# Kernel tuning notes

Measured on AMD Instinct MI355X. Metric: run time of the kernel, lower is better.

## Reference

```python
import jax, jax.numpy as jnp
import numpy as np

B, T, D = 256, 128, 64
H, A, O = 512, 128, 32


def setup_inputs() -> dict:
    key = jax.random.key(0)
    ks = jax.random.split(key, 16)
    u = lambda k, sh, lo, hi: jax.random.uniform(k, sh, jnp.float32, lo, hi)
    return {
        "x_states": jax.random.normal(ks[0], (B, T, D), jnp.float32),
        "x_dts": jax.random.uniform(ks[1], (B, T), jnp.float32) * 0.1,
        # StepwiseAttention params (stored [in, out])
        "Wq": u(ks[2], (D, A), -0.1, 0.1), "bq": u(ks[3], (A,), -0.1, 0.1),
        "Wk": u(ks[4], (H, A), -0.1, 0.1), "bk": u(ks[5], (A,), -0.1, 0.1),
        "Wv": u(ks[6], (H, A), -0.1, 0.1), "bv": u(ks[7], (A,), -0.1, 0.1),
        # LTCAttentionCell params
        "W_gd": u(ks[8], (D + H + A, 2 * H), -0.1, 0.1),
        "b_gd": u(ks[9], (2 * H,), -0.1, 0.1),
        "W_tau": u(ks[10], (H, H), -0.1, 0.1),
        "b_tau": u(ks[11], (H,), -0.1, 0.1),
        "gleak": u(ks[12], (H,), 0.001, 1.0),
        "cm": u(ks[13], (H,), 0.4, 0.6),
        # output head
        "W_fc": u(ks[14], (H, O), -0.1, 0.1),
        "b_fc": u(ks[15], (O,), -0.1, 0.1),
    }


def _forward(x_states, x_dts, Wq, bq, Wk, bk, Wv, bv,
             W_gd, b_gd, W_tau, b_tau, gleak, cm, W_fc, b_fc):
    scale = jnp.sqrt(jnp.asarray(A, jnp.float32))
    leak = jax.nn.softplus(cm) + jax.nn.softplus(gleak)  # [H]

    def dhdt(h, x_t, ctx):
        combined = jnp.concatenate([x_t, h, ctx], axis=1)        # [B, D+H+A]
        gd = combined @ W_gd + b_gd                              # [B, 2H]
        gate, dyn = jnp.split(gd, 2, axis=1)
        tau = jax.nn.softplus(h @ W_tau + b_tau)                 # [B, H]
        num = jax.nn.sigmoid(gate) * jnp.tanh(dyn) - h
        return num / (tau + leak + 1e-6)

    def step(carry, inp):
        h, hist = carry            # h [B,H], hist [B,T,H]
        t, x_t, dt = inp           # t scalar, x_t [B,D], dt [B]
        # stepwise attention over history h_1..h_t
        Q = x_t @ Wq + bq                                        # [B, A]
        K = hist @ Wk + bk                                       # [B, T, A]
        V = hist @ Wv + bv                                       # [B, T, A]
        scores = jnp.einsum('ba,bta->bt', Q, K) / scale          # [B, T]
        valid = jnp.arange(T) < t
        scores = jnp.where(valid[None, :], scores, -1e9)
        w = jax.nn.softmax(scores, axis=-1)
        ctx = jnp.einsum('bt,bta->ba', w, V)
        ctx = jnp.where(t > 0, ctx, jnp.zeros_like(ctx))         # empty history -> 0
        # one RK4 step (torchdiffeq 'rk4' = 3/8-rule variant), step size dt per sample
        dtc = dt[:, None]
        k1 = dhdt(h, x_t, ctx)
        k2 = dhdt(h + dtc * k1 / 3.0, x_t, ctx)
        k3 = dhdt(h + dtc * (k2 - k1 / 3.0), x_t, ctx)
        k4 = dhdt(h + dtc * (k1 - k2 + k3), x_t, ctx)
        h_next = h + dtc * (k1 + 3.0 * k2 + 3.0 * k3 + k4) / 8.0
        hist = jax.lax.dynamic_update_slice(hist, h_next[:, None, :], (0, t, 0))
        return (h_next, hist), None

    h0 = jnp.zeros((B, H), jnp.float32)
    hist0 = jnp.zeros((B, T, H), jnp.float32)
    xs = (jnp.arange(T), jnp.swapaxes(x_states, 0, 1), jnp.swapaxes(x_dts, 0, 1))
    (h_final, _), _ = jax.lax.scan(step, (h0, hist0), xs)
    return h_final @ W_fc + b_fc                                 # [B, O]


def reference(x_states, x_dts, Wq, bq, Wk, bk, Wv, bv,
              W_gd, b_gd, W_tau, b_tau, gleak, cm, W_fc, b_fc):
    return _forward(x_states, x_dts, Wq, bq, Wk, bk, Wv, bv,
                    W_gd, b_gd, W_tau, b_tau, gleak, cm, W_fc, b_fc)
```

## Files before the change

kernel.cpp:

```cpp
#include <hip/hip_runtime.h>
#include <math.h>

#define B_ 256
#define T_ 128
#define D_ 64
#define H_ 512
#define A_ 128
#define O_ 32

typedef __attribute__((ext_vector_type(8))) short short8;
typedef __attribute__((ext_vector_type(8))) unsigned short ushort8;
typedef __attribute__((ext_vector_type(4))) float floatx4;
typedef __attribute__((ext_vector_type(4))) unsigned int uintx4;
typedef unsigned long long ull;

__device__ __forceinline__ float sp_(float x) {
    return fmaxf(x, 0.f) + log1pf(expf(-fabsf(x)));
}
__device__ __forceinline__ float sigm_(float x) {
    return 1.f / (1.f + expf(-x));
}
__device__ __forceinline__ unsigned short f2bf_(float f) {
    unsigned int u = __float_as_uint(f);
    return (unsigned short)((u + 0x7FFFu + ((u >> 16) & 1u)) >> 16);
}
__device__ __forceinline__ float bf2f_(unsigned short u) {
    return __uint_as_float(((unsigned)u) << 16);
}

__device__ __forceinline__ void ld16sc(uintx4& d, const void* p) {
    asm volatile("global_load_dwordx4 %0, %1, off sc0 sc1"
                 : "=v"(d) : "v"(p) : "memory");
}
__device__ __forceinline__ void ld4sc(float& d, const void* p) {
    asm volatile("global_load_dword %0, %1, off sc0 sc1"
                 : "=v"(d) : "v"(p) : "memory");
}
__device__ __forceinline__ void ld4su(unsigned& d, const void* p) {
    asm volatile("global_load_dword %0, %1, off sc0 sc1"
                 : "=v"(d) : "v"(p) : "memory");
}
__device__ __forceinline__ void st64sc(ull* p, ull v) {
    asm volatile("global_store_dwordx2 %0, %1, off sc0 sc1"
                 :: "v"(p), "v"(v) : "memory");
}
__device__ __forceinline__ void stu32sc(unsigned* p, unsigned v) {
    asm volatile("global_store_dword %0, %1, off sc0 sc1"
                 :: "v"(p), "v"(v) : "memory");
}
__device__ __forceinline__ void vmwait4(uintx4& a, uintx4& b, uintx4& c,
                                        uintx4& d) {
    asm volatile("s_waitcnt vmcnt(0)"
                 : "+v"(a), "+v"(b), "+v"(c), "+v"(d)::"memory");
}
__device__ __forceinline__ void vmwait8(uintx4& a, uintx4& b, uintx4& c,
                                        uintx4& d, uintx4& e, uintx4& f,
                                        uintx4& g, uintx4& h) {
    asm volatile("s_waitcnt vmcnt(0)"
                 : "+v"(a), "+v"(b), "+v"(c), "+v"(d), "+v"(e), "+v"(f),
                   "+v"(g), "+v"(h)::"memory");
}
__device__ __forceinline__ void vmwait16f(float& a0, float& a1, float& a2,
                                          float& a3, float& a4, float& a5,
                                          float& a6, float& a7, float& b0,
                                          float& b1, float& b2, float& b3,
                                          float& b4, float& b5, float& b6,
                                          float& b7) {
    asm volatile("s_waitcnt vmcnt(0)"
                 : "+v"(a0), "+v"(a1), "+v"(a2), "+v"(a3), "+v"(a4), "+v"(a5),
                   "+v"(a6), "+v"(a7), "+v"(b0), "+v"(b1), "+v"(b2), "+v"(b3),
                   "+v"(b4), "+v"(b5), "+v"(b6), "+v"(b7)::"memory");
}
__device__ __forceinline__ void vmwait8u(unsigned& a, unsigned& b, unsigned& c,
                                         unsigned& d, unsigned& e, unsigned& f,
                                         unsigned& g, unsigned& h) {
    asm volatile("s_waitcnt vmcnt(0)"
                 : "+v"(a), "+v"(b), "+v"(c), "+v"(d), "+v"(e), "+v"(f),
                   "+v"(g), "+v"(h)::"memory");
}
__device__ __forceinline__ void vmwait4u(unsigned& a, unsigned& b, unsigned& c,
                                         unsigned& d) {
    asm volatile("s_waitcnt vmcnt(0)"
                 : "+v"(a), "+v"(b), "+v"(c), "+v"(d)::"memory");
}
__device__ __forceinline__ void vmwait1u(unsigned& a) {
    asm volatile("s_waitcnt vmcnt(0)" : "+v"(a)::"memory");
}
__device__ __forceinline__ floatx4 u2f_(uintx4 u) {
    union { uintx4 u; floatx4 f; } c;
    c.u = u;
    return c.f;
}
__device__ __forceinline__ void stf_(float* p, float v) {
    __hip_atomic_store(p, v, __ATOMIC_RELAXED, __HIP_MEMORY_SCOPE_SYSTEM);
}

__global__ void init_kernel(unsigned short* __restrict__ hpack,
                            unsigned* __restrict__ bar) {
    int i = blockIdx.x * 256 + threadIdx.x;
    if (i < B_ * H_) hpack[i] = 0;
    if (i < 18432) bar[i] = 0u;
}

__global__ void pack_w_kernel(const float* __restrict__ W_gd,
                              const float* __restrict__ W_tau,
                              const float* __restrict__ Wk,
                              const float* __restrict__ Wv,
                              unsigned short* __restrict__ Wpack) {
    int gid = blockIdx.x * 256 + threadIdx.x;
    if (gid >= 1114112) return;
    int j = gid & 7;
    int l = (gid >> 3) & 63;
    int kpart = (l >> 4) * 8 + j;
    int npart = l & 15;
    float v;
    if (gid < 786432) {
        int f = gid >> 9;
        int s = f % 3;
        int rem = f / 3;
        int kb = rem & 15, ct = rem >> 4;
        int k = kb * 32 + kpart;
        int c = ct * 16 + npart;
        if (s == 0)      v = W_gd[(size_t)(D_ + k) * 1024 + c];
        else if (s == 1) v = W_gd[(size_t)(D_ + k) * 1024 + 512 + c];
        else             v = W_tau[(size_t)k * 512 + c];
    } else if (gid < 851968) {
        int r = gid - 786432;
        int f = r >> 9;
        int s = f & 1, kb = (f >> 1) & 1, ct = f >> 2;
        int k = kb * 32 + kpart;
        int c = ct * 16 + npart;
        v = W_gd[(size_t)k * 1024 + s * 512 + c];
    } else if (gid < 983040) {
        int r = gid - 851968;
        int f = r >> 9;
        int s = f & 1, kb = (f >> 1) & 3, ct = f >> 3;
        int k = kb * 32 + kpart;
        int c = ct * 16 + npart;
        v = W_gd[(size_t)(D_ + H_ + k) * 1024 + s * 512 + c];
    } else {
        int r = gid - 983040;
        int f = r >> 9;
        int kb = f & 15, c4 = f >> 4;
        int k = kb * 32 + kpart;
        int n = (c4 & 7) * 16 + npart;
        v = (c4 < 8) ? Wk[(size_t)k * A_ + n] : Wv[(size_t)k * A_ + n];
    }
    Wpack[gid] = f2bf_(v);
}

__device__ __forceinline__ void gsyncF(unsigned* flags, int j, unsigned cnt) {
    asm volatile("s_waitcnt vmcnt(0)" ::: "memory");
    __syncthreads();
    if (threadIdx.x == 0) stu32sc(flags + j * 64, cnt);
    if (threadIdx.x < 8) {
        unsigned v;
        do {
            ld4su(v, flags + threadIdx.x * 64);
            vmwait1u(v);
            if (v >= cnt) break;
            __builtin_amdgcn_s_sleep(1);
        } while (true);
    }
    __syncthreads();
}

struct P {
    const float *x, *dts, *Wq, *bq, *bk, *bv, *b_gd, *b_tau, *gleak, *cm,
        *W_fc, *b_fc;
    float *h, *ctx, *out, *Kpart, *Vpart;
    unsigned short* Kh;
    const unsigned short *Wy, *Wx, *Wc, *Wkv;
    unsigned short *hpack, *yapack, *ybpack, *ycpack;
    unsigned* bar;
};

__global__ __launch_bounds__(256, 1) void fused_kernel(P p) {
    const int tid = threadIdx.x;
    const int bid = blockIdx.x;
    const int lane = tid & 63;
    const int wave = tid >> 6;
    const int g = bid & 15;
    const int j = bid >> 4;
    const int ct = j * 4 + wave;
    unsigned* flags = p.bar + g * 512;
    unsigned* senbase = p.bar + 8192;
    #define SEN(kind, src) (senbase + (((kind)*16 + g) * 8 + (src)) * 16)

    __shared__ float WqL[D_ * 129];
    __shared__ float xs4[2][D_];
    __shared__ float q4[2][A_];
    __shared__ float sc4[2][T_];
    __shared__ float red[2][2];
    __shared__ __align__(16) unsigned short AsL[32 * 256];
    __shared__ __align__(16) unsigned short ypbuf[4 * 256];
    __shared__ __align__(16) unsigned short As2[2 * 512];
    __shared__ unsigned short VhL[2][A_][136];

    const int quad = lane >> 4;
    const int c = ct * 16 + (lane & 15);
    const float btau = p.b_tau[c];
    const float lk = sp_(p.cm[c]) + sp_(p.gleak[c]) + 1e-6f;
    const float bgd_g = p.b_gd[c];
    const float bgd_d = p.b_gd[512 + c];
    const int aoff = (quad >> 1) * 256 + (lane & 15) * 16 + (quad & 1) * 8;
    const int ypw = wave * 256 + (lane & 15);

    const int sub = tid >> 7;
    const int tl = tid & 127;
    const int r = g * 16 + j * 2 + sub;
    const int rrow = r & 15;

    short8 wg[16], wd[16], wt[16];
    short8 wxg[2], wxd[2], wcg[4], wcd[4];
    {
        const short8* Wy8 = (const short8*)p.Wy;
        #pragma unroll
        for (int kb = 0; kb < 16; ++kb) {
            wg[kb] = Wy8[((ct * 16 + kb) * 3 + 0) * 64 + lane];
            wd[kb] = Wy8[((ct * 16 + kb) * 3 + 1) * 64 + lane];
            wt[kb] = Wy8[((ct * 16 + kb) * 3 + 2) * 64 + lane];
        }
        const short8* Wx8 = (const short8*)p.Wx;
        const short8* Wc8 = (const short8*)p.Wc;
        #pragma unroll
        for (int kb = 0; kb < 2; ++kb) {
            wxg[kb] = Wx8[((ct * 2 + kb) * 2 + 0) * 64 + lane];
            wxd[kb] = Wx8[((ct * 2 + kb) * 2 + 1) * 64 + lane];
        }
        #pragma unroll
        for (int kb = 0; kb < 4; ++kb) {
            wcg[kb] = Wc8[((ct * 4 + kb) * 2 + 0) * 64 + lane];
            wcd[kb] = Wc8[((ct * 4 + kb) * 2 + 1) * 64 + lane];
        }
    }

    for (int i = tid; i < D_ * A_; i += 256) {
        int d = i >> 7, a = i & 127;
        WqL[d * 129 + a] = p.Wq[i];
    }

    floatx4 hreg = {0.f, 0.f, 0.f, 0.f};
    floatx4 rk1, rk2, rk3, baseg, based, ycur, dt4;

    const short8* Wkv8 = (const short8*)p.Wkv;

    __syncthreads();

    for (int t = 0; t < T_; ++t) {
        {
            float kk[8], vv[8];
            uintx4 av[4];
            {
                const unsigned short* src = p.hpack + g * 8192;
                const unsigned expv = (unsigned)t;
                unsigned s0, s1, s2, s3, s4, s5, s6, s7;
                for (;;) {
                    #pragma unroll
                    for (int jj = 0; jj < 8; ++jj) {
                        ld4sc(kk[jj],
                              p.Kpart + ((g * 8 + jj) * 16 + rrow) * 128 + tl);
                        ld4sc(vv[jj],
                              p.Vpart + ((g * 8 + jj) * 16 + rrow) * 128 + tl);
                    }
                    #pragma unroll
                    for (int i = 0; i < 4; ++i)
                        ld16sc(av[i], src + (size_t)tid * 8 + i * 2048);
                    ld4su(s0, SEN(4, 0)); ld4su(s1, SEN(4, 1));
                    ld4su(s2, SEN(4, 2)); ld4su(s3, SEN(4, 3));
                    ld4su(s4, SEN(4, 4)); ld4su(s5, SEN(4, 5));
                    ld4su(s6, SEN(4, 6)); ld4su(s7, SEN(4, 7));
                    vmwait16f(kk[0], kk[1], kk[2], kk[3], kk[4], kk[5], kk[6],
                              kk[7], vv[0], vv[1], vv[2], vv[3], vv[4], vv[5],
                              vv[6], vv[7]);
                    vmwait4(av[0], av[1], av[2], av[3]);
                    vmwait8u(s0, s1, s2, s3, s4, s5, s6, s7);
                    if (s0 >= expv && s1 >= expv && s2 >= expv && s3 >= expv &&
                        s4 >= expv && s5 >= expv && s6 >= expv && s7 >= expv)
                        break;
                    __builtin_amdgcn_s_sleep(1);
                }
            }
            #pragma unroll
            for (int i = 0; i < 4; ++i)
                ((uintx4*)AsL)[tid + i * 256] = av[i];
            if (t > 0) {
                float ks = p.bk[tl], vs = p.bv[tl];
                #pragma unroll
                for (int jj = 0; jj < 8; ++jj) {
                    ks += kk[jj];
                    vs += vv[jj];
                }
                p.Kh[(size_t)(r * T_ + (t - 1)) * A_ + tl] = f2bf_(ks);
                VhL[sub][tl][t - 1] = f2bf_(vs);
            }
            if (tl < 16)
                ((float4*)xs4[sub])[tl] =
                    ((const float4*)&p.x[(r * T_ + t) * D_])[tl];
            __syncthreads();
            float qa = p.bq[tl];
            #pragma unroll 8
            for (int d = 0; d < D_; ++d) qa += xs4[sub][d] * WqL[d * 129 + tl];
            q4[sub][tl] = qa;
            __syncthreads();
            if (t == 0) {
                stf_(p.ctx + r * A_ + tl, 0.f);
            } else {
                const float rscale = 0.08838834764831845f;
                const int grp = tl >> 4, ln = tl & 15;
                float qv[8];
                #pragma unroll
                for (int i = 0; i < 8; ++i) qv[i] = q4[sub][ln * 8 + i];
                for (int s = grp; s < t; s += 8) {
                    ushort8 k8 = *((const ushort8*)(p.Kh +
                                     (size_t)(r * T_ + s) * A_) + ln);
                    float a2 = 0.f;
                    #pragma unroll
                    for (int i = 0; i < 8; ++i) a2 += bf2f_(k8[i]) * qv[i];
                    #pragma unroll
                    for (int off = 8; off > 0; off >>= 1)
                        a2 += __shfl_xor(a2, off, 16);
                    if (ln == 0) sc4[sub][s] = a2 * rscale;
                }
                __syncthreads();
                float mloc = -1e30f;
                for (int s = tl; s < t; s += 128)
                    mloc = fmaxf(mloc, sc4[sub][s]);
                #pragma unroll
                for (int off = 32; off > 0; off >>= 1)
                    mloc = fmaxf(mloc, __shfl_xor(mloc, off, 64));
                if (lane == 0) red[sub][wave & 1] = mloc;
                __syncthreads();
                float m = fmaxf(red[sub][0], red[sub][1]);
                float ssum = 0.f;
                for (int s = tl; s < t; s += 128) {
                    float e = expf(sc4[sub][s] - m);
                    sc4[sub][s] = e;
                    ssum += e;
                }
                #pragma unroll
                for (int off = 32; off > 0; off >>= 1)
                    ssum += __shfl_xor(ssum, off, 64);
                __syncthreads();
                if (lane == 0) red[sub][wave & 1] = ssum;
                __syncthreads();
                float rs = 1.f / (red[sub][0] + red[sub][1]);
                const unsigned short* Vrow = &VhL[sub][tl][0];
                float ca0 = 0.f, ca1 = 0.f;
                int s0 = 0;
                for (; s0 + 16 <= t; s0 += 16) {
                    ushort8 v0 = *(const ushort8*)(Vrow + s0);
                    ushort8 v1 = *(const ushort8*)(Vrow + s0 + 8);
                    #pragma unroll
                    for (int i = 0; i < 8; ++i) {
                        ca0 += sc4[sub][s0 + i] * bf2f_(v0[i]);
                        ca1 += sc4[sub][s0 + 8 + i] * bf2f_(v1[i]);
                    }
                }
                if (s0 + 8 <= t) {
                    ushort8 v0 = *(const ushort8*)(Vrow + s0);
                    #pragma unroll
                    for (int i = 0; i < 8; ++i)
                        ca0 += sc4[sub][s0 + i] * bf2f_(v0[i]);
                    s0 += 8;
                }
                for (; s0 < t; ++s0) ca0 += sc4[sub][s0] * bf2f_(Vrow[s0]);
                stf_(p.ctx + r * A_ + tl, (ca0 + ca1) * rs);
            }
        }
        asm volatile("s_waitcnt vmcnt(0)" ::: "memory");
        __syncthreads();
        if (tid == 0) stu32sc(SEN(0, j), (unsigned)(t + 1));

        {
            const int mrow = lane & 15;
            const float* crow = &p.ctx[(g * 16 + mrow) * A_];
            uintx4 cc[8];
            {
                const unsigned* senp = SEN(0, mrow >> 1);
                const unsigned expv = (unsigned)(t + 1);
                unsigned sv;
                for (;;) {
                    #pragma unroll
                    for (int kb = 0; kb < 4; ++kb) {
                        ld16sc(cc[2 * kb], crow + kb * 32 + quad * 8);
                        ld16sc(cc[2 * kb + 1], crow + kb * 32 + quad * 8 + 4);
                    }
                    ld4su(sv, senp);
                    vmwait8(cc[0], cc[1], cc[2], cc[3], cc[4], cc[5], cc[6],
                            cc[7]);
                    vmwait1u(sv);
                    if (sv >= expv) break;
                    __builtin_amdgcn_s_sleep(1);
                }
            }
            #pragma unroll
            for (int i = 0; i < 4; ++i)
                dt4[i] = p.dts[(g * 16 + quad * 4 + i) * T_ + t];

            floatx4 bg = {0.f, 0.f, 0.f, 0.f};
            floatx4 bd = {0.f, 0.f, 0.f, 0.f};
            const float4* xrow =
                (const float4*)&p.x[((g * 16 + mrow) * T_ + t) * D_];
            #pragma unroll
            for (int kb = 0; kb < 2; ++kb) {
                float4 u = xrow[kb * 8 + quad * 2], v = xrow[kb * 8 + quad * 2 + 1];
                short8 ax;
                ax[0] = (short)f2bf_(u.x); ax[1] = (short)f2bf_(u.y);
                ax[2] = (short)f2bf_(u.z); ax[3] = (short)f2bf_(u.w);
                ax[4] = (short)f2bf_(v.x); ax[5] = (short)f2bf_(v.y);
                ax[6] = (short)f2bf_(v.z); ax[7] = (short)f2bf_(v.w);
                bg = __builtin_amdgcn_mfma_f32_16x16x32_bf16(ax, wxg[kb], bg, 0, 0, 0);
                bd = __builtin_amdgcn_mfma_f32_16x16x32_bf16(ax, wxd[kb], bd, 0, 0, 0);
            }
            #pragma unroll
            for (int kb = 0; kb < 4; ++kb) {
                floatx4 f0 = u2f_(cc[2 * kb]), f1 = u2f_(cc[2 * kb + 1]);
                short8 ac;
                ac[0] = (short)f2bf_(f0[0]); ac[1] = (short)f2bf_(f0[1]);
                ac[2] = (short)f2bf_(f0[2]); ac[3] = (short)f2bf_(f0[3]);
                ac[4] = (short)f2bf_(f1[0]); ac[5] = (short)f2bf_(f1[1]);
                ac[6] = (short)f2bf_(f1[2]); ac[7] = (short)f2bf_(f1[3]);
                bg = __builtin_amdgcn_mfma_f32_16x16x32_bf16(ac, wcg[kb], bg, 0, 0, 0);
                bd = __builtin_amdgcn_mfma_f32_16x16x32_bf16(ac, wcd[kb], bd, 0, 0, 0);
            }
            floatx4 ag = {0.f, 0.f, 0.f, 0.f};
            floatx4 ad = {0.f, 0.f, 0.f, 0.f};
            floatx4 at = {0.f, 0.f, 0.f, 0.f};
            #pragma unroll
            for (int kb = 0; kb < 16; ++kb) {
                short8 a = *(const short8*)(AsL + kb * 512 + aoff);
                ag = __builtin_amdgcn_mfma_f32_16x16x32_bf16(a, wg[kb], ag, 0, 0, 0);
                ad = __builtin_amdgcn_mfma_f32_16x16x32_bf16(a, wd[kb], ad, 0, 0, 0);
                at = __builtin_amdgcn_mfma_f32_16x16x32_bf16(a, wt[kb], at, 0, 0, 0);
            }
            #pragma unroll
            for (int i = 0; i < 4; ++i) {
                baseg[i] = bg[i] + bgd_g;
                based[i] = bd[i] + bgd_d;
                float gate = ag[i] + baseg[i];
                float dyn = ad[i] + based[i];
                float tau = sp_(at[i] + btau);
                float ki = (sigm_(gate) * tanhf(dyn) - hreg[i]) / (tau + lk);
                rk1[i] = ki;
                float yn = hreg[i] + dt4[i] * ki * (1.f / 3.f);
                ycur[i] = yn;
                ypbuf[ypw + (quad * 4 + i) * 16] = f2bf_(yn);
            }
            __syncthreads();
            st64sc((ull*)p.yapack + g * 2048 + j * 256 + tid,
                   ((const ull*)ypbuf)[tid]);
        }
        asm volatile("s_waitcnt vmcnt(0)" ::: "memory");
        __syncthreads();
        if (tid == 0) stu32sc(SEN(1, j), (unsigned)(t + 1));

        #pragma unroll 1
        for (int stage = 2; stage <= 4; ++stage) {
            const unsigned short* ysrc =
                (stage == 2) ? p.yapack : (stage == 3) ? p.ybpack : p.ycpack;
            unsigned short* ydst =
                (stage == 2) ? p.ybpack : (stage == 3) ? p.ycpack : p.hpack;
            const int senk = stage - 1;
            {
                const unsigned short* src = ysrc + g * 8192;
                const unsigned expv = (unsigned)(t + 1);
                const int sb = tid >> 7;
                uintx4 av[4];
                unsigned s0, s1, s2, s3;
                for (;;) {
                    #pragma unroll
                    for (int i = 0; i < 4; ++i)
                        ld16sc(av[i], src + (size_t)tid * 8 + i * 2048);
                    ld4su(s0, SEN(senk, sb + 0));
                    ld4su(s1, SEN(senk, sb + 2));
                    ld4su(s2, SEN(senk, sb + 4));
                    ld4su(s3, SEN(senk, sb + 6));
                    vmwait4(av[0], av[1], av[2], av[3]);
                    vmwait4u(s0, s1, s2, s3);
                    if (s0 >= expv && s1 >= expv && s2 >= expv && s3 >= expv)
                        break;
                    __builtin_amdgcn_s_sleep(1);
                }
                #pragma unroll
                for (int i = 0; i < 4; ++i)
                    ((uintx4*)AsL)[tid + i * 256] = av[i];
            }
            __syncthreads();
            floatx4 ag = {0.f, 0.f, 0.f, 0.f};
            floatx4 ad = {0.f, 0.f, 0.f, 0.f};
            floatx4 at = {0.f, 0.f, 0.f, 0.f};
            #pragma unroll
            for (int kb = 0; kb < 16; ++kb) {
                short8 a = *(const short8*)(AsL + kb * 512 + aoff);
                ag = __builtin_amdgcn_mfma_f32_16x16x32_bf16(a, wg[kb], ag, 0, 0, 0);
                ad = __builtin_amdgcn_mfma_f32_16x16x32_bf16(a, wd[kb], ad, 0, 0, 0);
                at = __builtin_amdgcn_mfma_f32_16x16x32_bf16(a, wt[kb], at, 0, 0, 0);
            }
            const int lane_p = ((c >> 3) & 3) * 16;
            #pragma unroll
            for (int i = 0; i < 4; ++i) {
                float gate = ag[i] + baseg[i];
                float dyn = ad[i] + based[i];
                float tau = sp_(at[i] + btau);
                float ki = (sigm_(gate) * tanhf(dyn) - ycur[i]) / (tau + lk);
                float yn;
                if (stage == 2) {
                    rk2[i] = ki;
                    yn = hreg[i] + dt4[i] * (ki - rk1[i] * (1.f / 3.f));
                } else if (stage == 3) {
                    rk3[i] = ki;
                    yn = hreg[i] + dt4[i] * (rk1[i] - rk2[i] + ki);
                } else {
                    yn = hreg[i] +
                         dt4[i] * (rk1[i] + 3.f * rk2[i] + 3.f * rk3[i] + ki) * 0.125f;
                    hreg[i] = yn;
                }
                ycur[i] = yn;
                ypbuf[ypw + (quad * 4 + i) * 16] = f2bf_(yn);
                if (stage == 4)
                    As2[(wave >> 1) * 512 + (c & 7) +
                        (lane_p + quad * 4 + i) * 8] = f2bf_(yn);
            }
            __syncthreads();
            st64sc((ull*)ydst + g * 2048 + j * 256 + tid,
                   ((const ull*)ypbuf)[tid]);
            if (stage == 4) {
                #pragma unroll
                for (int h4 = 0; h4 < 4; ++h4) {
                    const int c4 = wave + h4 * 4;
                    floatx4 acc = {0.f, 0.f, 0.f, 0.f};
                    #pragma unroll
                    for (int kk2 = 0; kk2 < 2; ++kk2) {
                        short8 a = *(const short8*)(As2 + (kk2 * 64 + lane) * 8);
                        acc = __builtin_amdgcn_mfma_f32_16x16x32_bf16(
                            a, Wkv8[(c4 * 16 + (j * 2 + kk2)) * 64 + lane], acc,
                            0, 0, 0);
                    }
                    const int ac = (c4 & 7) * 16 + (lane & 15);
                    float* part = (c4 < 8) ? p.Kpart : p.Vpart;
                    #pragma unroll
                    for (int i = 0; i < 4; ++i)
                        stf_(part + ((g * 8 + j) * 16 + quad * 4 + i) * 128 + ac,
                             acc[i]);
                }
            }
            asm volatile("s_waitcnt vmcnt(0)" ::: "memory");
            __syncthreads();
            if (tid == 0) stu32sc(SEN(stage, j), (unsigned)(t + 1));
        }
    }

    #pragma unroll
    for (int i = 0; i < 4; ++i)
        stf_(p.h + (g * 16 + quad * 4 + i) * H_ + c, hreg[i]);
    gsyncF(flags, j, 1u);
    {
        const int o = tl & 31, ks = tl >> 5;
        float acc = 0.f;
        const float* hrow = p.h + r * H_ + ks * 128;
        const float* wcol = p.W_fc + ks * 128 * O_ + o;
        #pragma unroll 1
        for (int rd = 0; rd < 4; ++rd) {
            uintx4 hh[8];
            #pragma unroll
            for (int i = 0; i < 8; ++i)
                ld16sc(hh[i], hrow + rd * 32 + i * 4);
            vmwait8(hh[0], hh[1], hh[2], hh[3], hh[4], hh[5], hh[6], hh[7]);
            #pragma unroll
            for (int i = 0; i < 8; ++i) {
                floatx4 f = u2f_(hh[i]);
                #pragma unroll
                for (int e = 0; e < 4; ++e)
                    acc += f[e] * wcol[(rd * 32 + i * 4 + e) * O_];
            }
        }
        sc4[sub][tl] = acc;
        __syncthreads();
        if (ks == 0)
            p.out[r * O_ + o] = acc + sc4[sub][o + 32] + sc4[sub][o + 64] +
                                sc4[sub][o + 96] + p.b_fc[o];
    }
    #undef SEN
}

extern "C" void kernel_launch(void* const* d_in, const int* in_sizes, int n_in,
                              void* d_out, int out_size, void* d_ws,
                              size_t ws_size, hipStream_t stream) {
    (void)in_sizes; (void)n_in; (void)out_size; (void)ws_size;
    P p;
    p.x = (const float*)d_in[0];
    p.dts = (const float*)d_in[1];
    p.Wq = (const float*)d_in[2];
    p.bq = (const float*)d_in[3];
    const float* Wk = (const float*)d_in[4];
    p.bk = (const float*)d_in[5];
    const float* Wv = (const float*)d_in[6];
    p.bv = (const float*)d_in[7];
    const float* W_gd = (const float*)d_in[8];
    p.b_gd = (const float*)d_in[9];
    const float* W_tau = (const float*)d_in[10];
    p.b_tau = (const float*)d_in[11];
    p.gleak = (const float*)d_in[12];
    p.cm = (const float*)d_in[13];
    p.W_fc = (const float*)d_in[14];
    p.b_fc = (const float*)d_in[15];
    p.out = (float*)d_out;

    float* ws = (float*)d_ws;
    p.h = ws;
    p.ctx = p.h + B_ * H_;
    p.Kpart = p.ctx + B_ * A_;
    p.Vpart = p.Kpart + 262144;
    unsigned short* Wpack = (unsigned short*)(p.Vpart + 262144);
    p.Wy = Wpack;
    p.Wx = Wpack + 786432;
    p.Wc = Wpack + 851968;
    p.Wkv = Wpack + 983040;
    p.hpack = Wpack + 1114112;
    p.yapack = p.hpack + B_ * H_;
    p.ybpack = p.yapack + B_ * H_;
    p.ycpack = p.ybpack + B_ * H_;
    p.Kh = p.ycpack + B_ * H_;
    p.bar = (unsigned*)(p.Kh + (size_t)B_ * T_ * A_);

    init_kernel<<<512, 256, 0, stream>>>(p.hpack, p.bar);
    pack_w_kernel<<<4352, 256, 0, stream>>>(W_gd, W_tau, Wk, Wv, Wpack);

    fused_kernel<<<dim3(128), dim3(256), 0, stream>>>(p);
}
```

Before: 3.542 ms.

## Halve persistent block count with 512-thread blocks and move V history to global

The persistent fused kernel now runs 64 blocks of 512 threads (8 waves) instead of 128 blocks of 256, so each block owns twice as many hidden columns and batch rows. This halves the number of producer blocks that every consumer must poll through the sentinel flags and partial K/V buffers, which should cut the per-step cross-block synchronisation and reduction cost. To free LDS, the bf16 V history moves from shared memory to a global buffer, and the context sum reads it with strided scalar loads. That adds global traffic and latency in the attention loop, and fewer blocks means less total parallelism.

Result: slower. 8.395 ms (+137.0%).

```diff
diff --git a/kernel.cpp b/kernel.cpp
--- a/kernel.cpp
+++ b/kernel.cpp
@@ -48,10 +48,8 @@
     asm volatile("global_store_dword %0, %1, off sc0 sc1"
                  :: "v"(p), "v"(v) : "memory");
 }
-__device__ __forceinline__ void vmwait4(uintx4& a, uintx4& b, uintx4& c,
-                                        uintx4& d) {
-    asm volatile("s_waitcnt vmcnt(0)"
-                 : "+v"(a), "+v"(b), "+v"(c), "+v"(d)::"memory");
+__device__ __forceinline__ void vmwait2(uintx4& a, uintx4& b) {
+    asm volatile("s_waitcnt vmcnt(0)" : "+v"(a), "+v"(b)::"memory");
 }
 __device__ __forceinline__ void vmwait8(uintx4& a, uintx4& b, uintx4& c,
                                         uintx4& d, uintx4& e, uintx4& f,
@@ -60,28 +58,20 @@
                  : "+v"(a), "+v"(b), "+v"(c), "+v"(d), "+v"(e), "+v"(f),
                    "+v"(g), "+v"(h)::"memory");
 }
-__device__ __forceinline__ void vmwait16f(float& a0, float& a1, float& a2,
-                                          float& a3, float& a4, float& a5,
-                                          float& a6, float& a7, float& b0,
-                                          float& b1, float& b2, float& b3,
-                                          float& b4, float& b5, float& b6,
-                                          float& b7) {
+__device__ __forceinline__ void vmwait8f(float& a0, float& a1, float& a2,
+                                         float& a3, float& a4, float& a5,
+                                         float& a6, float& a7) {
     asm volatile("s_waitcnt vmcnt(0)"
                  : "+v"(a0), "+v"(a1), "+v"(a2), "+v"(a3), "+v"(a4), "+v"(a5),
-                   "+v"(a6), "+v"(a7), "+v"(b0), "+v"(b1), "+v"(b2), "+v"(b3),
-                   "+v"(b4), "+v"(b5), "+v"(b6), "+v"(b7)::"memory");
-}
-__device__ __forceinline__ void vmwait8u(unsigned& a, unsigned& b, unsigned& c,
-                                         unsigned& d, unsigned& e, unsigned& f,
-                                         unsigned& g, unsigned& h) {
-    asm volatile("s_waitcnt vmcnt(0)"
-                 : "+v"(a), "+v"(b), "+v"(c), "+v"(d), "+v"(e), "+v"(f),
-                   "+v"(g), "+v"(h)::"memory");
+                   "+v"(a6), "+v"(a7)::"memory");
 }
 __device__ __forceinline__ void vmwait4u(unsigned& a, unsigned& b, unsigned& c,
                                          unsigned& d) {
     asm volatile("s_waitcnt vmcnt(0)"
                  : "+v"(a), "+v"(b), "+v"(c), "+v"(d)::"memory");
+}
+__device__ __forceinline__ void vmwait2u(unsigned& a, unsigned& b) {
+    asm volatile("s_waitcnt vmcnt(0)" : "+v"(a), "+v"(b)::"memory");
 }
 __device__ __forceinline__ void vmwait1u(unsigned& a) {
     asm volatile("s_waitcnt vmcnt(0)" : "+v"(a)::"memory");
@@ -153,7 +143,7 @@
     asm volatile("s_waitcnt vmcnt(0)" ::: "memory");
     __syncthreads();
     if (threadIdx.x == 0) stu32sc(flags + j * 64, cnt);
-    if (threadIdx.x < 8) {
+    if (threadIdx.x < 4) {
         unsigned v;
         do {
             ld4su(v, flags + threadIdx.x * 64);
@@ -169,33 +159,32 @@
     const float *x, *dts, *Wq, *bq, *bk, *bv, *b_gd, *b_tau, *gleak, *cm,
         *W_fc, *b_fc;
     float *h, *ctx, *out, *Kpart, *Vpart;
-    unsigned short* Kh;
+    unsigned short *Kh, *Vh;
     const unsigned short *Wy, *Wx, *Wc, *Wkv;
     unsigned short *hpack, *yapack, *ybpack, *ycpack;
     unsigned* bar;
 };
 
-__global__ __launch_bounds__(256, 1) void fused_kernel(P p) {
+__global__ __launch_bounds__(512, 2) void fused_kernel(P p) {
     const int tid = threadIdx.x;
     const int bid = blockIdx.x;
     const int lane = tid & 63;
     const int wave = tid >> 6;
     const int g = bid & 15;
     const int j = bid >> 4;
-    const int ct = j * 4 + wave;
+    const int ct = j * 8 + wave;
     unsigned* flags = p.bar + g * 512;
     unsigned* senbase = p.bar + 8192;
     #define SEN(kind, src) (senbase + (((kind)*16 + g) * 8 + (src)) * 16)
 
     __shared__ float WqL[D_ * 129];
-    __shared__ float xs4[2][D_];
-    __shared__ float q4[2][A_];
-    __shared__ float sc4[2][T_];
-    __shared__ float red[2][2];
+    __shared__ float xs4[4][D_];
+    __shared__ float q4[4][A_];
+    __shared__ float sc4[4][T_];
+    __shared__ float red[4][2];
     __shared__ __align__(16) unsigned short AsL[32 * 256];
-    __shared__ __align__(16) unsigned short ypbuf[4 * 256];
-    __shared__ __align__(16) unsigned short As2[2 * 512];
-    __shared__ unsigned short VhL[2][A_][136];
+    __shared__ __align__(16) unsigned short ypbuf[8 * 256];
+    __shared__ __align__(16) unsigned short As2[4 * 512];
 
     const int quad = lane >> 4;
     const int c = ct * 16 + (lane & 15);
@@ -208,7 +197,7 @@
 
     const int sub = tid >> 7;
     const int tl = tid & 127;
-    const int r = g * 16 + j * 2 + sub;
+    const int r = g * 16 + j * 4 + sub;
     const int rrow = r & 15;
 
     short8 wg[16], wd[16], wt[16];
@@ -235,7 +224,7 @@
         }
     }
 
-    for (int i = tid; i < D_ * A_; i += 256) {
+    for (int i = tid; i < D_ * A_; i += 512) {
         int d = i >> 7, a = i & 127;
         WqL[d * 129 + a] = p.Wq[i];
     }
@@ -249,50 +238,46 @@
 
     for (int t = 0; t < T_; ++t) {
         {
-            float kk[8], vv[8];
-            uintx4 av[4];
+            float kk[4], vv[4];
+            uintx4 av[2];
             {
                 const unsigned short* src = p.hpack + g * 8192;
                 const unsigned expv = (unsigned)t;
-                unsigned s0, s1, s2, s3, s4, s5, s6, s7;
+                unsigned s0, s1, s2, s3;
                 for (;;) {
                     #pragma unroll
-                    for (int jj = 0; jj < 8; ++jj) {
+                    for (int jj = 0; jj < 4; ++jj) {
                         ld4sc(kk[jj],
-                              p.Kpart + ((g * 8 + jj) * 16 + rrow) * 128 + tl);
+                              p.Kpart + ((g * 4 + jj) * 16 + rrow) * 128 + tl);
                         ld4sc(vv[jj],
-                              p.Vpart + ((g * 8 + jj) * 16 + rrow) * 128 + tl);
+                              p.Vpart + ((g * 4 + jj) * 16 + rrow) * 128 + tl);
                     }
                     #pragma unroll
-                    for (int i = 0; i < 4; ++i)
-                        ld16sc(av[i], src + (size_t)tid * 8 + i * 2048);
+                    for (int i = 0; i < 2; ++i)
+                        ld16sc(av[i], src + (size_t)tid * 8 + i * 4096);
                     ld4su(s0, SEN(4, 0)); ld4su(s1, SEN(4, 1));
                     ld4su(s2, SEN(4, 2)); ld4su(s3, SEN(4, 3));
-                    ld4su(s4, SEN(4, 4)); ld4su(s5, SEN(4, 5));
-                    ld4su(s6, SEN(4, 6)); ld4su(s7, SEN(4, 7));
-                    vmwait16f(kk[0], kk[1], kk[2], kk[3], kk[4], kk[5], kk[6],
-                              kk[7], vv[0], vv[1], vv[2], vv[3], vv[4], vv[5],
-                              vv[6], vv[7]);
-                    vmwait4(av[0], av[1], av[2], av[3]);
-                    vmwait8u(s0, s1, s2, s3, s4, s5, s6, s7);
-                    if (s0 >= expv && s1 >= expv && s2 >= expv && s3 >= expv &&
-                        s4 >= expv && s5 >= expv && s6 >= expv && s7 >= expv)
+                    vmwait8f(kk[0], kk[1], kk[2], kk[3], vv[0], vv[1], vv[2],
+                             vv[3]);
+                    vmwait2(av[0], av[1]);
+                    vmwait4u(s0, s1, s2, s3);
+                    if (s0 >= expv && s1 >= expv && s2 >= expv && s3 >= expv)
                         break;
                     __builtin_amdgcn_s_sleep(1);
                 }
             }
             #pragma unroll
-            for (int i = 0; i < 4; ++i)
-                ((uintx4*)AsL)[tid + i * 256] = av[i];
+            for (int i = 0; i < 2; ++i)
+                ((uintx4*)AsL)[tid + i * 512] = av[i];
             if (t > 0) {
                 float ks = p.bk[tl], vs = p.bv[tl];
                 #pragma unroll
-                for (int jj = 0; jj < 8; ++jj) {
+                for (int jj = 0; jj < 4; ++jj) {
                     ks += kk[jj];
                     vs += vv[jj];
                 }
                 p.Kh[(size_t)(r * T_ + (t - 1)) * A_ + tl] = f2bf_(ks);
-                VhL[sub][tl][t - 1] = f2bf_(vs);
+                p.Vh[(size_t)(r * T_ + (t - 1)) * A_ + tl] = f2bf_(vs);
             }
             if (tl < 16)
                 ((float4*)xs4[sub])[tl] =
@@ -345,26 +330,14 @@
                 if (lane == 0) red[sub][wave & 1] = ssum;
                 __syncthreads();
                 float rs = 1.f / (red[sub][0] + red[sub][1]);
-                const unsigned short* Vrow = &VhL[sub][tl][0];
+                const unsigned short* Vb = p.Vh + (size_t)r * T_ * A_ + tl;
                 float ca0 = 0.f, ca1 = 0.f;
-                int s0 = 0;
-                for (; s0 + 16 <= t; s0 += 16) {
-                    ushort8 v0 = *(const ushort8*)(Vrow + s0);
-                    ushort8 v1 = *(const ushort8*)(Vrow + s0 + 8);
-                    #pragma unroll
-                    for (int i = 0; i < 8; ++i) {
-                        ca0 += sc4[sub][s0 + i] * bf2f_(v0[i]);
-                        ca1 += sc4[sub][s0 + 8 + i] * bf2f_(v1[i]);
-                    }
-                }
-                if (s0 + 8 <= t) {
-                    ushort8 v0 = *(const ushort8*)(Vrow + s0);
-                    #pragma unroll
-                    for (int i = 0; i < 8; ++i)
-                        ca0 += sc4[sub][s0 + i] * bf2f_(v0[i]);
-                    s0 += 8;
-                }
-                for (; s0 < t; ++s0) ca0 += sc4[sub][s0] * bf2f_(Vrow[s0]);
+                int sv = 0;
+                for (; sv + 2 <= t; sv += 2) {
+                    ca0 += sc4[sub][sv] * bf2f_(Vb[(size_t)sv * A_]);
+                    ca1 += sc4[sub][sv + 1] * bf2f_(Vb[(size_t)(sv + 1) * A_]);
+                }
+                if (sv < t) ca0 += sc4[sub][sv] * bf2f_(Vb[(size_t)sv * A_]);
                 stf_(p.ctx + r * A_ + tl, (ca0 + ca1) * rs);
             }
         }
@@ -377,7 +350,7 @@
             const float* crow = &p.ctx[(g * 16 + mrow) * A_];
             uintx4 cc[8];
             {
-                const unsigned* senp = SEN(0, mrow >> 1);
+                const unsigned* senp = SEN(0, mrow >> 2);
                 const unsigned expv = (unsigned)(t + 1);
                 unsigned sv;
                 for (;;) {
@@ -448,7 +421,7 @@
                 ypbuf[ypw + (quad * 4 + i) * 16] = f2bf_(yn);
             }
             __syncthreads();
-            st64sc((ull*)p.yapack + g * 2048 + j * 256 + tid,
+            st64sc((ull*)p.yapack + g * 2048 + j * 512 + tid,
                    ((const ull*)ypbuf)[tid]);
         }
         asm volatile("s_waitcnt vmcnt(0)" ::: "memory");
@@ -465,26 +438,23 @@
             {
                 const unsigned short* src = ysrc + g * 8192;
                 const unsigned expv = (unsigned)(t + 1);
-                const int sb = tid >> 7;
-                uintx4 av[4];
-                unsigned s0, s1, s2, s3;
+                const int sb = tid >> 8;
+                uintx4 av[2];
+                unsigned s0, s1;
                 for (;;) {
                     #pragma unroll
-                    for (int i = 0; i < 4; ++i)
-                        ld16sc(av[i], src + (size_t)tid * 8 + i * 2048);
-                    ld4su(s0, SEN(senk, sb + 0));
+                    for (int i = 0; i < 2; ++i)
+                        ld16sc(av[i], src + (size_t)tid * 8 + i * 4096);
+                    ld4su(s0, SEN(senk, sb));
                     ld4su(s1, SEN(senk, sb + 2));
-                    ld4su(s2, SEN(senk, sb + 4));
-                    ld4su(s3, SEN(senk, sb + 6));
-                    vmwait4(av[0], av[1], av[2], av[3]);
-                    vmwait4u(s0, s1, s2, s3);
-                    if (s0 >= expv && s1 >= expv && s2 >= expv && s3 >= expv)
-                        break;
+                    vmwait2(av[0], av[1]);
+                    vmwait2u(s0, s1);
+                    if (s0 >= expv && s1 >= expv) break;
                     __builtin_amdgcn_s_sleep(1);
                 }
                 #pragma unroll
-                for (int i = 0; i < 4; ++i)
-                    ((uintx4*)AsL)[tid + i * 256] = av[i];
+                for (int i = 0; i < 2; ++i)
+                    ((uintx4*)AsL)[tid + i * 512] = av[i];
             }
             __syncthreads();
             floatx4 ag = {0.f, 0.f, 0.f, 0.f};
@@ -523,25 +493,25 @@
                         (lane_p + quad * 4 + i) * 8] = f2bf_(yn);
             }
             __syncthreads();
-            st64sc((ull*)ydst + g * 2048 + j * 256 + tid,
+            st64sc((ull*)ydst + g * 2048 + j * 512 + tid,
                    ((const ull*)ypbuf)[tid]);
             if (stage == 4) {
                 #pragma unroll
-                for (int h4 = 0; h4 < 4; ++h4) {
-                    const int c4 = wave + h4 * 4;
+                for (int h4 = 0; h4 < 2; ++h4) {
+                    const int c4 = wave + h4 * 8;
                     floatx4 acc = {0.f, 0.f, 0.f, 0.f};
                     #pragma unroll
-                    for (int kk2 = 0; kk2 < 2; ++kk2) {
+                    for (int kk2 = 0; kk2 < 4; ++kk2) {
                         short8 a = *(const short8*)(As2 + (kk2 * 64 + lane) * 8);
                         acc = __builtin_amdgcn_mfma_f32_16x16x32_bf16(
-                            a, Wkv8[(c4 * 16 + (j * 2 + kk2)) * 64 + lane], acc,
+                            a, Wkv8[(c4 * 16 + (j * 4 + kk2)) * 64 + lane], acc,
                             0, 0, 0);
                     }
                     const int ac = (c4 & 7) * 16 + (lane & 15);
                     float* part = (c4 < 8) ? p.Kpart : p.Vpart;
                     #pragma unroll
                     for (int i = 0; i < 4; ++i)
-                        stf_(part + ((g * 8 + j) * 16 + quad * 4 + i) * 128 + ac,
+                        stf_(part + ((g * 4 + j) * 16 + quad * 4 + i) * 128 + ac,
                              acc[i]);
                 }
             }
@@ -611,8 +581,8 @@
     p.h = ws;
     p.ctx = p.h + B_ * H_;
     p.Kpart = p.ctx + B_ * A_;
-    p.Vpart = p.Kpart + 262144;
-    unsigned short* Wpack = (unsigned short*)(p.Vpart + 262144);
+    p.Vpart = p.Kpart + 131072;
+    unsigned short* Wpack = (unsigned short*)(p.Vpart + 131072);
     p.Wy = Wpack;
     p.Wx = Wpack + 786432;
     p.Wc = Wpack + 851968;
@@ -622,10 +592,11 @@
     p.ybpack = p.yapack + B_ * H_;
     p.ycpack = p.ybpack + B_ * H_;
     p.Kh = p.ycpack + B_ * H_;
-    p.bar = (unsigned*)(p.Kh + (size_t)B_ * T_ * A_);
+    p.Vh = p.Kh + (size_t)B_ * T_ * A_;
+    p.bar = (unsigned*)(p.Vh + (size_t)B_ * T_ * A_);
 
     init_kernel<<<512, 256, 0, stream>>>(p.hpack, p.bar);
     pack_w_kernel<<<4352, 256, 0, stream>>>(W_gd, W_tau, Wk, Wv, Wpack);
 
-    fused_kernel<<<dim3(128), dim3(256), 0, stream>>>(p);
-}
+    fused_kernel<<<dim3(64), dim3(512), 0, stream>>>(p);
+}
```
